# Performance work log

Measured on AMD Instinct MI355X. Metric: run time of the kernel, lower is better.

The kernel has to match this reference:

```python
import jax, jax.numpy as jnp
import numpy as np

F = 128          # num_features
NRBF = 20        # num_rbf_features
N_NODES = 25000
N_EDGES = 400000


def setup_inputs() -> dict:
    key = jax.random.key(0)
    ks = jax.random.split(key, 12)
    inp = {
        "idx_i": jax.random.randint(ks[0], (N_EDGES,), 0, N_NODES, dtype=jnp.int32),
        "idx_j": jax.random.randint(ks[1], (N_EDGES,), 0, N_NODES, dtype=jnp.int32),
        "rel_dir": jax.random.normal(ks[2], (N_EDGES, 3), dtype=jnp.float32),
        "rel_dist_cut": jax.random.uniform(ks[3], (N_EDGES,), dtype=jnp.float32),
        "rbf_features": jax.random.normal(ks[4], (N_EDGES, NRBF), dtype=jnp.float32),
        "scalar_features": jax.random.normal(ks[5], (N_NODES, F), dtype=jnp.float32),
        "vector_features": jax.random.normal(ks[6], (N_NODES, F, 3), dtype=jnp.float32),
        # scalar_network: Linear(F,F) -> SiLU -> Linear(F,3F)
        "W1": jax.random.normal(ks[7], (F, F), dtype=jnp.float32) / np.sqrt(F),
        "b1": jnp.zeros((F,), dtype=jnp.float32),
        "W2": jax.random.normal(ks[8], (3 * F, F), dtype=jnp.float32) / np.sqrt(F),
        "b2": jnp.zeros((3 * F,), dtype=jnp.float32),
        # rbf_network: Linear(NRBF, 3F)
        "Wr": jax.random.normal(ks[9], (3 * F, NRBF), dtype=jnp.float32) / np.sqrt(NRBF),
        "br": jnp.zeros((3 * F,), dtype=jnp.float32),
    }
    return inp


def reference(idx_i, idx_j, rel_dir, rel_dist_cut, rbf_features,
              scalar_features, vector_features, W1, b1, W2, b2, Wr, br):
    n_nodes = scalar_features.shape[0]
    # phi: per-node MLP -> [N, 3F]
    h = jax.nn.silu(scalar_features @ W1.T + b1)
    phi = h @ W2.T + b2
    # W: RBF-derived edge weights gated by cosine-cut distance -> [E, 3F]
    W = (rbf_features @ Wr.T + br) * rel_dist_cut[:, None]
    phi_W = phi[idx_j] * W                                  # [E, 3F]
    phi_W_vv, phi_W_ss, phi_W_vs = jnp.split(phi_W, 3, axis=-1)
    # scatter-add scalar residuals
    scalar_res = jax.ops.segment_sum(phi_W_ss, idx_i, num_segments=n_nodes)
    # per-edge vector messages [E, F, 3]
    vec_per_edge = (vector_features[idx_j] * phi_W_vv[..., None]
                    + phi_W_vs[..., None] * rel_dir[:, None, :])
    vector_res = jax.ops.segment_sum(vec_per_edge, idx_i, num_segments=n_nodes)
    return scalar_features + scalar_res, vector_features + vector_res
```

## Files before the change

kernel.cpp:

```cpp
#include <hip/hip_runtime.h>
#include <hip/hip_fp16.h>

#define F 128
#define F3 384
#define NRBF 20
#define NPB 16
#define CHUNK 64

typedef unsigned int u32;
typedef _Float16 half8 __attribute__((ext_vector_type(8)));
typedef float floatx4 __attribute__((ext_vector_type(4)));

__device__ __forceinline__ float2 uph(u32 u) {
    __half2 h = *(__half2*)&u;
    return __half22float2(h);
}
__device__ __forceinline__ u32 pkh(float a, float b) {
    __half2 h = __floats2half2_rn(a, b);
    return *(u32*)&h;
}

__device__ __forceinline__ float fdot2f(u32 a, u32 b, float c) {
#if defined(__has_builtin)
#if __has_builtin(__builtin_amdgcn_fdot2)
    typedef _Float16 h2 __attribute__((ext_vector_type(2)));
    return __builtin_amdgcn_fdot2(*(h2*)&a, *(h2*)&b, c, false);
#else
    float2 fa = uph(a), fb = uph(b);
    return fmaf(fa.x, fb.x, fmaf(fa.y, fb.y, c));
#endif
#else
    float2 fa = uph(a), fb = uph(b);
    return fmaf(fa.x, fb.x, fmaf(fa.y, fb.y, c));
#endif
}

__global__ void prep_kernel(const float* __restrict__ Wr,
                            const float* __restrict__ W1, const float* __restrict__ W2,
                            u32* __restrict__ WrTh, _Float16* __restrict__ Wh,
                            int* __restrict__ counts, int n_nodes) {
    int t = blockIdx.x * blockDim.x + threadIdx.x;
    if (t < 10 * F3) {
        int rr = t / F3, f = t % F3;
        WrTh[rr * F3 + f] = pkh(Wr[f * NRBF + 2 * rr], Wr[f * NRBF + 2 * rr + 1]);
        return;
    }
    int u = t - 10 * F3;
    if (u < (F + F3) * F) {
        int n = u >> 7, k = u & (F - 1);
        float w = (n < F) ? W1[n * F + k] : W2[(size_t)(n - F) * F + k];
        Wh[u] = (_Float16)w;
        return;
    }
    int z = u - (F + F3) * F;
    if (z < n_nodes) counts[z] = 0;
}

__launch_bounds__(256)
__global__ void fusedB2_kernel(const float* __restrict__ sf,
                               const _Float16* __restrict__ Wh,
                               const float* __restrict__ b1, const float* __restrict__ b2,
                               const float* __restrict__ vf, __half* __restrict__ gbufh,
                               const int* __restrict__ idx_i, int* __restrict__ counts,
                               int n_nodes, int n_edges, int PHB) {
    __shared__ _Float16 hl[4][16][136];
    int blk = blockIdx.x, tid = threadIdx.x;

    if (blk >= PHB) {
        int e = (blk - PHB) * 256 + tid;
        if (e < n_edges) atomicAdd(&counts[idx_i[e]], 1);
        return;
    }

    int lane = tid & 63;
    int wv = tid >> 6;
    int col = lane & 15;
    int kg = lane >> 4;
    int row0 = blk * 64 + wv * 16;

    half8 a1[4];
#pragma unroll
    for (int kb = 0; kb < 4; kb++) {
        int rr = row0 + col;
        if (rr >= n_nodes) rr = n_nodes - 1;
        const float4* xp = (const float4*)(sf + (size_t)rr * F + kb * 32 + kg * 8);
        float4 x0 = xp[0], x1 = xp[1];
        half8 a;
        a[0] = (_Float16)x0.x; a[1] = (_Float16)x0.y; a[2] = (_Float16)x0.z; a[3] = (_Float16)x0.w;
        a[4] = (_Float16)x1.x; a[5] = (_Float16)x1.y; a[6] = (_Float16)x1.z; a[7] = (_Float16)x1.w;
        a1[kb] = a;
    }

    floatx4 acc[8];
#pragma unroll
    for (int nt = 0; nt < 8; nt++) acc[nt] = (floatx4){0.f, 0.f, 0.f, 0.f};
#pragma unroll
    for (int nt = 0; nt < 8; nt++) {
#pragma unroll
        for (int kb = 0; kb < 4; kb++) {
            half8 b = *(const half8*)(Wh + (size_t)(nt * 16 + col) * F + kb * 32 + kg * 8);
            acc[nt] = __builtin_amdgcn_mfma_f32_16x16x32_f16(a1[kb], b, acc[nt], 0, 0, 0);
        }
    }
#pragma unroll
    for (int nt = 0; nt < 8; nt++) {
        int f1 = nt * 16 + col;
        float bb = b1[f1];
#pragma unroll
        for (int r = 0; r < 4; r++) {
            float v = acc[nt][r] + bb;
            float s = v / (1.f + __expf(-v));
            hl[wv][kg * 4 + r][f1] = (_Float16)s;
        }
    }

    half8 a2[4];
#pragma unroll
    for (int kb = 0; kb < 4; kb++)
        a2[kb] = *(const half8*)&hl[wv][col][kb * 32 + kg * 8];

#pragma unroll
    for (int c = 0; c < 3; c++) {
#pragma unroll
        for (int nt = 0; nt < 8; nt++) acc[nt] = (floatx4){0.f, 0.f, 0.f, 0.f};
#pragma unroll
        for (int nt = 0; nt < 8; nt++) {
#pragma unroll
            for (int kb = 0; kb < 4; kb++) {
                half8 b = *(const half8*)(Wh + (size_t)(F + c * 128 + nt * 16 + col) * F + kb * 32 + kg * 8);
                acc[nt] = __builtin_amdgcn_mfma_f32_16x16x32_f16(a2[kb], b, acc[nt], 0, 0, 0);
            }
        }
#pragma unroll
        for (int nt = 0; nt < 8; nt++) {
            int f2 = c * 128 + nt * 16 + col;
            float bb = b2[f2];
            int slot = (f2 & 63) * 12 + ((f2 >> 6) & 1) * 6 + (f2 >> 7);
#pragma unroll
            for (int r = 0; r < 4; r++) {
                int node = row0 + kg * 4 + r;
                if (node < n_nodes)
                    gbufh[(size_t)node * 768 + slot] = __float2half(acc[nt][r] + bb);
            }
        }
    }

    int base = blk * 64;
    for (int idx = tid; idx < 64 * 64; idx += 256) {
        int nl = idx >> 6, ln = idx & 63;
        int node = base + nl;
        if (node < n_nodes) {
            const float* v = vf + (size_t)node * F3;
            u32* gp = (u32*)(gbufh + (size_t)node * 768 + ln * 12);
            float a0 = v[ln * 3 + 0], a1v = v[ln * 3 + 1], a2v = v[ln * 3 + 2];
            float c0 = v[(ln + 64) * 3 + 0], c1 = v[(ln + 64) * 3 + 1], c2 = v[(ln + 64) * 3 + 2];
            ((__half*)gp)[3] = __float2half(a0);
            gp[2] = pkh(a1v, a2v);
            ((__half*)gp)[9] = __float2half(c0);
            gp[5] = pkh(c1, c2);
        }
    }
}

#define SCAN_T 1024
#define SCAN_MAXN 25600
__launch_bounds__(SCAN_T)
__global__ void scan_lds_kernel(const int* __restrict__ counts, int* __restrict__ row_start,
                                int* __restrict__ cursor, int n) {
    __shared__ int sbuf[SCAN_MAXN];
    __shared__ int partial[SCAN_T];
    int t = threadIdx.x;
    for (int i = t; i < n; i += SCAN_T) sbuf[i] = counts[i];
    __syncthreads();
    int C = (n + SCAN_T - 1) / SCAN_T;
    int beg = t * C, end = min(beg + C, n);
    int sum = 0;
    for (int i = beg; i < end; i++) sum += sbuf[i];
    partial[t] = sum;
    __syncthreads();
    for (int off = 1; off < SCAN_T; off <<= 1) {
        int v = (t >= off) ? partial[t - off] : 0;
        __syncthreads();
        partial[t] += v;
        __syncthreads();
    }
    int base = (t == 0) ? 0 : partial[t - 1];
    for (int i = beg; i < end; i++) { int c = sbuf[i]; sbuf[i] = base; base += c; }
    __syncthreads();
    for (int i = t; i < n; i += SCAN_T) { int v = sbuf[i]; row_start[i] = v; cursor[i] = v; }
    if (t == SCAN_T - 1) row_start[n] = partial[SCAN_T - 1];
}

__launch_bounds__(1024)
__global__ void scan_kernel(const int* __restrict__ counts, int* __restrict__ row_start,
                            int* __restrict__ cursor, int n) {
    __shared__ int partial[1024];
    int t = threadIdx.x;
    int C = (n + 1023) / 1024;
    int beg = t * C, end = min(beg + C, n);
    int sum = 0;
    for (int i = beg; i < end; i++) sum += counts[i];
    partial[t] = sum;
    __syncthreads();
    for (int off = 1; off < 1024; off <<= 1) {
        int v = (t >= off) ? partial[t - off] : 0;
        __syncthreads();
        partial[t] += v;
        __syncthreads();
    }
    int base = (t == 0) ? 0 : partial[t - 1];
    for (int i = beg; i < end; i++) {
        int c = counts[i];
        row_start[i] = base; cursor[i] = base; base += c;
    }
    if (t == 1023) row_start[n] = partial[1023];
}

__global__ void build_records(const int* __restrict__ idx_i, const int* __restrict__ idx_j,
                              const float* __restrict__ rel_dir, const float* __restrict__ rdc,
                              const float* __restrict__ rbf, int* __restrict__ cursor,
                              u32* __restrict__ recs, int n_edges) {
    int e = blockIdx.x * blockDim.x + threadIdx.x;
    if (e >= n_edges) return;
    int p = atomicAdd(&cursor[idx_i[e]], 1);
    u32 r[16];
    r[0] = (u32)idx_j[e];
    r[1] = __float_as_uint(rdc[e]);
    r[2] = __float_as_uint(rel_dir[e * 3 + 0]);
    r[3] = __float_as_uint(rel_dir[e * 3 + 1]);
    r[4] = __float_as_uint(rel_dir[e * 3 + 2]);
    const float* rb = rbf + (size_t)e * NRBF;
#pragma unroll
    for (int t = 0; t < 10; t++) r[5 + t] = pkh(rb[2 * t], rb[2 * t + 1]);
    r[15] = 0;
    float4* dst = (float4*)(recs + (size_t)p * 16);
    const float4* src = (const float4*)r;
    dst[0] = src[0]; dst[1] = src[1]; dst[2] = src[2]; dst[3] = src[3];
}

__global__ void scatter_kernel(const int* __restrict__ idx_i, int* __restrict__ cursor,
                               int* __restrict__ edge_order, int n_edges) {
    int e = blockIdx.x * blockDim.x + threadIdx.x;
    if (e < n_edges) {
        int p = atomicAdd(&cursor[idx_i[e]], 1);
        edge_order[p] = e;
    }
}

__launch_bounds__(256)
__global__ void gather5_kernel(const float* __restrict__ sf, const float* __restrict__ vf,
                               const u32* __restrict__ WrTh, const float* __restrict__ br,
                               const u32* __restrict__ gbuf, const u32* __restrict__ recs,
                               const int* __restrict__ row_start,
                               float* __restrict__ out_s, float* __restrict__ out_v,
                               int n_nodes) {
    __shared__ u32 lsm[4][CHUNK * 16];
    int tid = threadIdx.x;
    int lane = tid & 63;
    int wvid = tid >> 6;
    int w = wvid & 1;
    int node = blockIdx.x * 2 + (wvid >> 1);
    if (node >= n_nodes) return;
    u32* lds = lsm[wvid];

    int fb = lane + 64 * w;
    u32 wrpk[3][10];
    float brv[3];
#pragma unroll
    for (int k = 0; k < 3; k++) {
        brv[k] = br[fb + 128 * k];
#pragma unroll
        for (int rr = 0; rr < 10; rr++)
            wrpk[k][rr] = WrTh[rr * F3 + fb + 128 * k];
    }

    float acc_s = 0.f, av0 = 0.f, av1 = 0.f, av2 = 0.f;
    int beg = row_start[node];
    int end = row_start[node + 1];

    for (int cb = beg; cb < end; cb += CHUNK) {
        int cnt = min(CHUNK, end - cb);
        {
            const float4* src = (const float4*)(recs + (size_t)cb * 16);
            int nf4 = cnt * 4;
            for (int t = lane; t < nf4; t += 64)
                ((float4*)lds)[t] = src[t];
        }

        auto issueL = [&](u32& g0, u32& g1, u32& g2, int m) {
            if (m < cnt) {
                int j = (int)lds[m * 16];
                const u32* gp = gbuf + (size_t)j * 384 + lane * 6 + w * 3;
                g0 = gp[0]; g1 = gp[1]; g2 = gp[2];
            }
        };
        auto computeE = [&](u32 g0, u32 g1, u32 g2, int m) {
            const uint4* q = (const uint4*)(lds + m * 16);
            uint4 q0 = q[0], q1 = q[1], q2 = q[2], q3 = q[3];
            float rd = __uint_as_float(q0.y);
            float dx = __uint_as_float(q0.z);
            float dy = __uint_as_float(q0.w);
            float dz = __uint_as_float(q1.x);
            u32 rbu[10] = { q1.y, q1.z, q1.w, q2.x, q2.y, q2.z, q2.w, q3.x, q3.y, q3.z };
            float W0 = brv[0], W1f = brv[1], W2f = brv[2];
#pragma unroll
            for (int rr = 0; rr < 10; rr++) {
                W0  = fdot2f(rbu[rr], wrpk[0][rr], W0);
                W1f = fdot2f(rbu[rr], wrpk[1][rr], W1f);
                W2f = fdot2f(rbu[rr], wrpk[2][rr], W2f);
            }
            float2 p01  = uph(g0);
            float2 p2v0 = uph(g1);
            float2 v12  = uph(g2);
            float pw0 = W0  * rd * p01.x;
            float pw1 = W1f * rd * p01.y;
            float pw2 = W2f * rd * p2v0.x;
            acc_s += pw1;
            av0 += p2v0.y * pw0 + pw2 * dx;
            av1 += v12.x  * pw0 + pw2 * dy;
            av2 += v12.y  * pw0 + pw2 * dz;
        };

        u32 A0, A1, A2, B0, B1, B2, C0, C1, C2, D0, D1, D2;
        issueL(A0, A1, A2, 0); issueL(B0, B1, B2, 1);
        issueL(C0, C1, C2, 2); issueL(D0, D1, D2, 3);
        int m = 0;
        while (true) {
            if (m >= cnt) break; computeE(A0, A1, A2, m); m++; issueL(A0, A1, A2, m + 3);
            if (m >= cnt) break; computeE(B0, B1, B2, m); m++; issueL(B0, B1, B2, m + 3);
            if (m >= cnt) break; computeE(C0, C1, C2, m); m++; issueL(C0, C1, C2, m + 3);
            if (m >= cnt) break; computeE(D0, D1, D2, m); m++; issueL(D0, D1, D2, m + 3);
        }
    }

    out_s[(size_t)node * F + fb] = sf[(size_t)node * F + fb] + acc_s;
    const float* vfi = vf + (size_t)node * F3 + fb * 3;
    float* ovi = out_v + (size_t)node * F3 + fb * 3;
    ovi[0] = vfi[0] + av0;
    ovi[1] = vfi[1] + av1;
    ovi[2] = vfi[2] + av2;
}

__launch_bounds__(256)
__global__ void gather3_kernel(const int* __restrict__ idx_j,
                               const float* __restrict__ rel_dir, const float* __restrict__ rdc,
                               const float* __restrict__ rbf,
                               const float* __restrict__ sf, const float* __restrict__ vf,
                               const u32* __restrict__ WrTh, const float* __restrict__ br,
                               const u32* __restrict__ gbuf,
                               const int* __restrict__ row_start, const int* __restrict__ edge_order,
                               float* __restrict__ out_s, float* __restrict__ out_v,
                               int n_nodes) {
    int lane = threadIdx.x & 63;
    int w = (threadIdx.x >> 6) & 1;
    int node = blockIdx.x * 2 + (threadIdx.x >> 7);
    if (node >= n_nodes) return;

    int fb = lane + 64 * w;
    u32 wrpk[3][10];
    float brv[3];
#pragma unroll
    for (int k = 0; k < 3; k++) {
        brv[k] = br[fb + 128 * k];
#pragma unroll
        for (int rr = 0; rr < 10; rr++)
            wrpk[k][rr] = WrTh[rr * F3 + fb + 128 * k];
    }

    float acc_s = 0.f, av0 = 0.f, av1 = 0.f, av2 = 0.f;
    int beg = row_start[node];
    int end = row_start[node + 1];

    for (int cb = beg; cb < end; cb += 64) {
        int cnt = min(64, end - cb);
        int jv = 0; float rdv = 0.f, dxv = 0.f, dyv = 0.f, dzv = 0.f;
        u32 rbm[10];
#pragma unroll
        for (int rr = 0; rr < 10; rr++) rbm[rr] = 0;
        if (lane < cnt) {
            int e = edge_order[cb + lane];
            jv = idx_j[e];
            rdv = rdc[e];
            dxv = rel_dir[e * 3 + 0]; dyv = rel_dir[e * 3 + 1]; dzv = rel_dir[e * 3 + 2];
            const float4* rp = (const float4*)(rbf + (size_t)e * NRBF);
            float4 r0 = rp[0], r1 = rp[1], r2 = rp[2], r3 = rp[3], r4 = rp[4];
            rbm[0] = pkh(r0.x, r0.y); rbm[1] = pkh(r0.z, r0.w);
            rbm[2] = pkh(r1.x, r1.y); rbm[3] = pkh(r1.z, r1.w);
            rbm[4] = pkh(r2.x, r2.y); rbm[5] = pkh(r2.z, r2.w);
            rbm[6] = pkh(r3.x, r3.y); rbm[7] = pkh(r3.z, r3.w);
            rbm[8] = pkh(r4.x, r4.y); rbm[9] = pkh(r4.z, r4.w);
        }
        auto issue = [&](u32& g0, u32& g1, u32& g2, int k) {
            int j = __shfl(jv, k, 64);
            const u32* gp = gbuf + (size_t)j * 384 + lane * 6 + w * 3;
            g0 = gp[0]; g1 = gp[1]; g2 = gp[2];
        };
        auto compute = [&](u32 g0, u32 g1, u32 g2, int k) {
            float rd = __shfl(rdv, k, 64);
            float dx = __shfl(dxv, k, 64);
            float dy = __shfl(dyv, k, 64);
            float dz = __shfl(dzv, k, 64);
            float W0 = brv[0], W1f = brv[1], W2f = brv[2];
#pragma unroll
            for (int rr = 0; rr < 10; rr++) {
                u32 rbi = (u32)__shfl((int)rbm[rr], k, 64);
                W0  = fdot2f(rbi, wrpk[0][rr], W0);
                W1f = fdot2f(rbi, wrpk[1][rr], W1f);
                W2f = fdot2f(rbi, wrpk[2][rr], W2f);
            }
            float2 p01 = uph(g0);
            float2 p2v0 = uph(g1);
            float2 v12 = uph(g2);
            float pw0 = W0 * rd * p01.x;
            float pw1 = W1f * rd * p01.y;
            float pw2 = W2f * rd * p2v0.x;
            acc_s += pw1;
            av0 += p2v0.y * pw0 + pw2 * dx;
            av1 += v12.x  * pw0 + pw2 * dy;
            av2 += v12.y  * pw0 + pw2 * dz;
        };
        u32 A0, A1, A2, B0, B1, B2;
        issue(A0, A1, A2, 0);
        int k = 0;
        while (k + 2 <= cnt) {
            issue(B0, B1, B2, k + 1);
            compute(A0, A1, A2, k);
            if (k + 2 < cnt) issue(A0, A1, A2, k + 2);
            compute(B0, B1, B2, k + 1);
            k += 2;
        }
        if (k < cnt) compute(A0, A1, A2, k);
    }

    out_s[(size_t)node * F + fb] = sf[(size_t)node * F + fb] + acc_s;
    const float* vfi = vf + (size_t)node * F3 + fb * 3;
    float* ovi = out_v + (size_t)node * F3 + fb * 3;
    ovi[0] = vfi[0] + av0;
    ovi[1] = vfi[1] + av1;
    ovi[2] = vfi[2] + av2;
}

__global__ void transpose_wr(const float* __restrict__ Wr, float* __restrict__ WrT) {
    int idx = blockIdx.x * blockDim.x + threadIdx.x;
    if (idx < F3 * NRBF) {
        int f = idx / NRBF, r = idx % NRBF;
        WrT[r * F3 + f] = Wr[idx];
    }
}

__global__ void init_out(const float* __restrict__ sf, const float* __restrict__ vf,
                         float* __restrict__ out, int n_scalar, int n_total) {
    int i = blockIdx.x * blockDim.x + threadIdx.x;
    int n4 = n_total >> 2;
    if (i < n4) {
        float4 v;
        int base = i << 2;
        if (base < n_scalar) v = ((const float4*)sf)[i];
        else                 v = ((const float4*)vf)[i - (n_scalar >> 2)];
        ((float4*)out)[i] = v;
    }
}

__launch_bounds__(256)
__global__ void phi32_kernel(const float* __restrict__ sf,
                             const float* __restrict__ W1, const float* __restrict__ b1,
                             const float* __restrict__ W2, const float* __restrict__ b2,
                             float* __restrict__ phi, int n_nodes) {
    __shared__ float xs[NPB][F];
    __shared__ float hs[NPB][F];
    int tid = threadIdx.x;
    int nb = blockIdx.x * NPB;
    for (int t = tid; t < NPB * F / 4; t += 256) {
        int n  = t / (F / 4);
        int k4 = t % (F / 4);
        float4 v = make_float4(0.f, 0.f, 0.f, 0.f);
        if (nb + n < n_nodes) v = ((const float4*)(sf + (size_t)(nb + n) * F))[k4];
        ((float4*)&xs[n][0])[k4] = v;
    }
    __syncthreads();
    {
        int f = tid & (F - 1);
        int half_ = tid >> 7;
        float acc[8];
#pragma unroll
        for (int nn = 0; nn < 8; nn++) acc[nn] = 0.f;
        const float* w1row = W1 + (size_t)f * F;
        for (int k = 0; k < F; k++) {
            float w = w1row[k];
#pragma unroll
            for (int nn = 0; nn < 8; nn++)
                acc[nn] += xs[half_ * 8 + nn][k] * w;
        }
        float b = b1[f];
#pragma unroll
        for (int nn = 0; nn < 8; nn++) {
            float v = acc[nn] + b;
            hs[half_ * 8 + nn][f] = v / (1.f + __expf(-v));
        }
    }
    __syncthreads();
    for (int f = tid; f < F3; f += 256) {
        float acc[NPB];
#pragma unroll
        for (int n = 0; n < NPB; n++) acc[n] = 0.f;
        const float* w2row = W2 + (size_t)f * F;
        for (int k = 0; k < F; k++) {
            float w = w2row[k];
#pragma unroll
            for (int n = 0; n < NPB; n++)
                acc[n] += hs[n][k] * w;
        }
        float b = b2[f];
        for (int n = 0; n < NPB; n++)
            if (nb + n < n_nodes)
                phi[(size_t)(nb + n) * F3 + f] = acc[n] + b;
    }
}

__launch_bounds__(256)
__global__ void edge_kernel(const int* __restrict__ idx_i, const int* __restrict__ idx_j,
                            const float* __restrict__ rel_dir, const float* __restrict__ rdc,
                            const float* __restrict__ rbf,
                            const float* __restrict__ vf,
                            const float* __restrict__ WrT, const float* __restrict__ br,
                            const float* __restrict__ phi,
                            float* __restrict__ out_s, float* __restrict__ out_v,
                            int n_edges) {
    int lane = threadIdx.x & 63;
    int e = (int)((blockIdx.x * (unsigned)blockDim.x + threadIdx.x) >> 6);
    if (e >= n_edges) return;
    int i = idx_i[e], j = idx_j[e];
    float rd = rdc[e];
    float d0 = rel_dir[e * 3 + 0], d1 = rel_dir[e * 3 + 1], d2 = rel_dir[e * 3 + 2];
    float rb[NRBF];
#pragma unroll
    for (int r = 0; r < NRBF; r++) rb[r] = rbf[(size_t)e * NRBF + r];
    const float* pj = phi + (size_t)j * F3;
    float pw[6];
#pragma unroll
    for (int q = 0; q < 6; q++) {
        int f = lane + 64 * q;
        float acc = br[f];
#pragma unroll
        for (int r = 0; r < NRBF; r++)
            acc += rb[r] * WrT[r * F3 + f];
        pw[q] = acc * rd * pj[f];
    }
    atomicAdd(&out_s[(size_t)i * F + lane],       pw[2]);
    atomicAdd(&out_s[(size_t)i * F + lane + 64],  pw[3]);
    const float* vfj = vf + (size_t)j * F * 3;
    float* ovi = out_v + (size_t)i * F * 3;
#pragma unroll
    for (int h = 0; h < 2; h++) {
        int f = lane + 64 * h;
        float vv = pw[h];
        float vs = pw[4 + h];
        atomicAdd(&ovi[f * 3 + 0], vfj[f * 3 + 0] * vv + vs * d0);
        atomicAdd(&ovi[f * 3 + 1], vfj[f * 3 + 1] * vv + vs * d1);
        atomicAdd(&ovi[f * 3 + 2], vfj[f * 3 + 2] * vv + vs * d2);
    }
}

extern "C" void kernel_launch(void* const* d_in, const int* in_sizes, int n_in,
                              void* d_out, int out_size, void* d_ws, size_t ws_size,
                              hipStream_t stream) {
    const int*   idx_i   = (const int*)d_in[0];
    const int*   idx_j   = (const int*)d_in[1];
    const float* rel_dir = (const float*)d_in[2];
    const float* rdc     = (const float*)d_in[3];
    const float* rbf     = (const float*)d_in[4];
    const float* sf      = (const float*)d_in[5];
    const float* vf      = (const float*)d_in[6];
    const float* W1      = (const float*)d_in[7];
    const float* b1      = (const float*)d_in[8];
    const float* W2      = (const float*)d_in[9];
    const float* b2      = (const float*)d_in[10];
    const float* Wr      = (const float*)d_in[11];
    const float* br      = (const float*)d_in[12];

    int E = in_sizes[0];
    int N = in_sizes[5] / F;

    float* out_s = (float*)d_out;
    float* out_v = out_s + (size_t)N * F;

    size_t off = 0;
    auto slab = [&](size_t bytes) { size_t o = off; off = (off + bytes + 255) & ~(size_t)255; return o; };
    size_t o_wrth = slab((size_t)10 * F3 * sizeof(u32));
    size_t o_wh   = slab((size_t)(F + F3) * F * sizeof(_Float16));
    size_t o_gbuf = slab((size_t)N * 768 * sizeof(__half));
    size_t o_cnt  = slab((size_t)N * sizeof(int));
    size_t o_row  = slab((size_t)(N + 1) * sizeof(int));
    size_t o_rec  = slab((size_t)E * 64);
    size_t need_v5 = off;

    size_t off3 = 0;
    auto slab3 = [&](size_t bytes) { size_t o = off3; off3 = (off3 + bytes + 255) & ~(size_t)255; return o; };
    size_t t_wrth = slab3((size_t)10 * F3 * sizeof(u32));
    size_t t_wh   = slab3((size_t)(F + F3) * F * sizeof(_Float16));
    size_t t_gbuf = slab3((size_t)N * 768 * sizeof(__half));
    size_t t_cnt  = slab3((size_t)N * sizeof(int));
    size_t t_row  = slab3((size_t)(N + 1) * sizeof(int));
    size_t t_ord  = slab3((size_t)E * sizeof(int));
    size_t need_v3 = off3;

    int prep_threads = 10 * F3 + (F + F3) * F + N;
    int HB = (E + 255) / 256;
    int PHB = (N + 63) / 64;

    if (ws_size >= need_v5) {
        u32*      WrTh      = (u32*)((char*)d_ws + o_wrth);
        _Float16* Wh        = (_Float16*)((char*)d_ws + o_wh);
        __half*   gbufh     = (__half*)((char*)d_ws + o_gbuf);
        u32*      gbuf      = (u32*)gbufh;
        int*      counts    = (int*)((char*)d_ws + o_cnt);
        int*      cursor    = counts;
        int*      row_start = (int*)((char*)d_ws + o_row);
        u32*      recs      = (u32*)((char*)d_ws + o_rec);

        prep_kernel<<<(prep_threads + 255) / 256, 256, 0, stream>>>(Wr, W1, W2, WrTh, Wh, counts, N);
        fusedB2_kernel<<<PHB + HB, 256, 0, stream>>>(sf, Wh, b1, b2, vf, gbufh,
                                                     idx_i, counts, N, E, PHB);
        if (N <= SCAN_MAXN)
            scan_lds_kernel<<<1, SCAN_T, 0, stream>>>(counts, row_start, cursor, N);
        else
            scan_kernel<<<1, 1024, 0, stream>>>(counts, row_start, cursor, N);
        build_records<<<(E + 255) / 256, 256, 0, stream>>>(idx_i, idx_j, rel_dir, rdc, rbf,
                                                           cursor, recs, E);
        gather5_kernel<<<(N + 1) / 2, 256, 0, stream>>>(sf, vf, WrTh, br, gbuf, recs,
                                                        row_start, out_s, out_v, N);
    } else if (ws_size >= need_v3) {
        u32*      WrTh      = (u32*)((char*)d_ws + t_wrth);
        _Float16* Wh        = (_Float16*)((char*)d_ws + t_wh);
        __half*   gbufh     = (__half*)((char*)d_ws + t_gbuf);
        u32*      gbuf      = (u32*)gbufh;
        int*      counts    = (int*)((char*)d_ws + t_cnt);
        int*      cursor    = counts;
        int*      row_start = (int*)((char*)d_ws + t_row);
        int*      edge_ord  = (int*)((char*)d_ws + t_ord);

        prep_kernel<<<(prep_threads + 255) / 256, 256, 0, stream>>>(Wr, W1, W2, WrTh, Wh, counts, N);
        fusedB2_kernel<<<PHB + HB, 256, 0, stream>>>(sf, Wh, b1, b2, vf, gbufh,
                                                     idx_i, counts, N, E, PHB);
        if (N <= SCAN_MAXN)
            scan_lds_kernel<<<1, SCAN_T, 0, stream>>>(counts, row_start, cursor, N);
        else
            scan_kernel<<<1, 1024, 0, stream>>>(counts, row_start, cursor, N);
        scatter_kernel<<<(E + 255) / 256, 256, 0, stream>>>(idx_i, cursor, edge_ord, E);
        gather3_kernel<<<(N + 1) / 2, 256, 0, stream>>>(idx_j, rel_dir, rdc, rbf, sf, vf,
                                                        WrTh, br, gbuf, row_start, edge_ord,
                                                        out_s, out_v, N);
    } else {
        size_t off2 = 0;
        auto slab2 = [&](size_t bytes) { size_t o = off2; off2 = (off2 + bytes + 255) & ~(size_t)255; return o; };
        size_t f_wrt = slab2((size_t)F3 * NRBF * sizeof(float));
        size_t f_phi = slab2((size_t)N * F3 * sizeof(float));
        float* WrT = (float*)((char*)d_ws + f_wrt);
        float* phi = (float*)((char*)d_ws + f_phi);

        int n_scalar = N * F;
        int n_total  = N * F * 4;
        init_out<<<(n_total / 4 + 255) / 256, 256, 0, stream>>>(sf, vf, (float*)d_out, n_scalar, n_total);
        transpose_wr<<<(F3 * NRBF + 255) / 256, 256, 0, stream>>>(Wr, WrT);
        phi32_kernel<<<(N + NPB - 1) / NPB, 256, 0, stream>>>(sf, W1, b1, W2, b2, phi, N);
        edge_kernel<<<(E + 3) / 4, 256, 0, stream>>>(idx_i, idx_j, rel_dir, rdc, rbf,
                                                     vf, WrT, br, phi, out_s, out_v, E);
    }
}
```

Baseline: 233.6 us.

## Process each node with one wavefront covering two features per lane

The gather kernel now assigns one 64-lane wavefront per destination node instead of two. Each lane handles features lane and lane+64, so the per-edge record in LDS and the edge loop are shared across twice the work. Each lane now issues 8-byte gbuf loads instead of 4-byte ones, and the edge-record LDS copy is done once per node instead of twice. In exchange, register pressure roughly doubles (60 packed Wr weights per lane), which may reduce occupancy, and there are half as many wavefronts to hide gather latency.

Result: slower. 260.8 us (+11.6%).

```diff
diff --git a/kernel.cpp b/kernel.cpp
--- a/kernel.cpp
+++ b/kernel.cpp
@@ -247,8 +247,10 @@
     }
 }
 
+struct Gb { uint2 a, b, c; };
+
 __launch_bounds__(256)
-__global__ void gather5_kernel(const float* __restrict__ sf, const float* __restrict__ vf,
+__global__ void gather6_kernel(const float* __restrict__ sf, const float* __restrict__ vf,
                                const u32* __restrict__ WrTh, const float* __restrict__ br,
                                const u32* __restrict__ gbuf, const u32* __restrict__ recs,
                                const int* __restrict__ row_start,
@@ -258,23 +260,28 @@
     int tid = threadIdx.x;
     int lane = tid & 63;
     int wvid = tid >> 6;
-    int w = wvid & 1;
-    int node = blockIdx.x * 2 + (wvid >> 1);
+    int node = blockIdx.x * 4 + wvid;
     if (node >= n_nodes) return;
     u32* lds = lsm[wvid];
 
-    int fb = lane + 64 * w;
-    u32 wrpk[3][10];
-    float brv[3];
-#pragma unroll
-    for (int k = 0; k < 3; k++) {
-        brv[k] = br[fb + 128 * k];
-#pragma unroll
-        for (int rr = 0; rr < 10; rr++)
-            wrpk[k][rr] = WrTh[rr * F3 + fb + 128 * k];
-    }
-
-    float acc_s = 0.f, av0 = 0.f, av1 = 0.f, av2 = 0.f;
+    u32 wrpk[6][10];
+    float brv[6];
+    {
+        const int fofs[6] = { 0, 128, 256, 64, 192, 320 };
+#pragma unroll
+        for (int k = 0; k < 6; k++) {
+            int f = lane + fofs[k];
+            brv[k] = br[f];
+#pragma unroll
+            for (int rr = 0; rr < 10; rr++)
+                wrpk[k][rr] = WrTh[rr * F3 + f];
+        }
+    }
+
+    float accs0 = 0.f, accs1 = 0.f;
+    float avA0 = 0.f, avA1 = 0.f, avA2 = 0.f;
+    float avB0 = 0.f, avB1 = 0.f, avB2 = 0.f;
+
     int beg = row_start[node];
     int end = row_start[node + 1];
 
@@ -287,14 +294,16 @@
                 ((float4*)lds)[t] = src[t];
         }
 
-        auto issueL = [&](u32& g0, u32& g1, u32& g2, int m) {
+        auto issueL = [&](Gb& g, int m) {
             if (m < cnt) {
                 int j = (int)lds[m * 16];
-                const u32* gp = gbuf + (size_t)j * 384 + lane * 6 + w * 3;
-                g0 = gp[0]; g1 = gp[1]; g2 = gp[2];
+                const u32* gp = gbuf + (size_t)j * 384 + lane * 6;
+                g.a = *(const uint2*)gp;
+                g.b = *(const uint2*)(gp + 2);
+                g.c = *(const uint2*)(gp + 4);
             }
         };
-        auto computeE = [&](u32 g0, u32 g1, u32 g2, int m) {
+        auto computeE = [&](const Gb& g, int m) {
             const uint4* q = (const uint4*)(lds + m * 16);
             uint4 q0 = q[0], q1 = q[1], q2 = q[2], q3 = q[3];
             float rd = __uint_as_float(q0.y);
@@ -302,43 +311,57 @@
             float dy = __uint_as_float(q0.w);
             float dz = __uint_as_float(q1.x);
             u32 rbu[10] = { q1.y, q1.z, q1.w, q2.x, q2.y, q2.z, q2.w, q3.x, q3.y, q3.z };
-            float W0 = brv[0], W1f = brv[1], W2f = brv[2];
-#pragma unroll
-            for (int rr = 0; rr < 10; rr++) {
-                W0  = fdot2f(rbu[rr], wrpk[0][rr], W0);
-                W1f = fdot2f(rbu[rr], wrpk[1][rr], W1f);
-                W2f = fdot2f(rbu[rr], wrpk[2][rr], W2f);
+            float W[6];
+#pragma unroll
+            for (int k = 0; k < 6; k++) {
+                float acc = brv[k];
+#pragma unroll
+                for (int rr = 0; rr < 10; rr++)
+                    acc = fdot2f(rbu[rr], wrpk[k][rr], acc);
+                W[k] = acc * rd;
             }
-            float2 p01  = uph(g0);
-            float2 p2v0 = uph(g1);
-            float2 v12  = uph(g2);
-            float pw0 = W0  * rd * p01.x;
-            float pw1 = W1f * rd * p01.y;
-            float pw2 = W2f * rd * p2v0.x;
-            acc_s += pw1;
-            av0 += p2v0.y * pw0 + pw2 * dx;
-            av1 += v12.x  * pw0 + pw2 * dy;
-            av2 += v12.y  * pw0 + pw2 * dz;
+            float2 pA = uph(g.a.x);
+            float2 pB = uph(g.a.y);
+            float2 pC = uph(g.b.x);
+            float2 pD = uph(g.b.y);
+            float2 pE = uph(g.c.x);
+            float2 pF = uph(g.c.y);
+            float pwvA = W[0] * pA.x, pwsA = W[1] * pA.y, pwxA = W[2] * pB.x;
+            float pwvB = W[3] * pD.x, pwsB = W[4] * pD.y, pwxB = W[5] * pE.x;
+            accs0 += pwsA;
+            accs1 += pwsB;
+            avA0 += pB.y * pwvA + pwxA * dx;
+            avA1 += pC.x * pwvA + pwxA * dy;
+            avA2 += pC.y * pwvA + pwxA * dz;
+            avB0 += pE.y * pwvB + pwxB * dx;
+            avB1 += pF.x * pwvB + pwxB * dy;
+            avB2 += pF.y * pwvB + pwxB * dz;
         };
 
-        u32 A0, A1, A2, B0, B1, B2, C0, C1, C2, D0, D1, D2;
-        issueL(A0, A1, A2, 0); issueL(B0, B1, B2, 1);
-        issueL(C0, C1, C2, 2); issueL(D0, D1, D2, 3);
+        Gb A, B, C, D;
+        issueL(A, 0); issueL(B, 1); issueL(C, 2); issueL(D, 3);
         int m = 0;
         while (true) {
-            if (m >= cnt) break; computeE(A0, A1, A2, m); m++; issueL(A0, A1, A2, m + 3);
-            if (m >= cnt) break; computeE(B0, B1, B2, m); m++; issueL(B0, B1, B2, m + 3);
-            if (m >= cnt) break; computeE(C0, C1, C2, m); m++; issueL(C0, C1, C2, m + 3);
-            if (m >= cnt) break; computeE(D0, D1, D2, m); m++; issueL(D0, D1, D2, m + 3);
-        }
-    }
-
-    out_s[(size_t)node * F + fb] = sf[(size_t)node * F + fb] + acc_s;
-    const float* vfi = vf + (size_t)node * F3 + fb * 3;
-    float* ovi = out_v + (size_t)node * F3 + fb * 3;
-    ovi[0] = vfi[0] + av0;
-    ovi[1] = vfi[1] + av1;
-    ovi[2] = vfi[2] + av2;
+            if (m >= cnt) break; computeE(A, m); m++; issueL(A, m + 3);
+            if (m >= cnt) break; computeE(B, m); m++; issueL(B, m + 3);
+            if (m >= cnt) break; computeE(C, m); m++; issueL(C, m + 3);
+            if (m >= cnt) break; computeE(D, m); m++; issueL(D, m + 3);
+        }
+    }
+
+    const float* sfi = sf + (size_t)node * F;
+    float* osi = out_s + (size_t)node * F;
+    osi[lane]      = sfi[lane]      + accs0;
+    osi[lane + 64] = sfi[lane + 64] + accs1;
+
+    const float* vfi = vf + (size_t)node * F3;
+    float* ovi = out_v + (size_t)node * F3;
+    ovi[lane * 3 + 0] = vfi[lane * 3 + 0] + avA0;
+    ovi[lane * 3 + 1] = vfi[lane * 3 + 1] + avA1;
+    ovi[lane * 3 + 2] = vfi[lane * 3 + 2] + avA2;
+    ovi[(lane + 64) * 3 + 0] = vfi[(lane + 64) * 3 + 0] + avB0;
+    ovi[(lane + 64) * 3 + 1] = vfi[(lane + 64) * 3 + 1] + avB1;
+    ovi[(lane + 64) * 3 + 2] = vfi[(lane + 64) * 3 + 2] + avB2;
 }
 
 __launch_bounds__(256)
@@ -627,7 +650,7 @@
             scan_kernel<<<1, 1024, 0, stream>>>(counts, row_start, cursor, N);
         build_records<<<(E + 255) / 256, 256, 0, stream>>>(idx_i, idx_j, rel_dir, rdc, rbf,
                                                            cursor, recs, E);
-        gather5_kernel<<<(N + 1) / 2, 256, 0, stream>>>(sf, vf, WrTh, br, gbuf, recs,
+        gather6_kernel<<<(N + 3) / 4, 256, 0, stream>>>(sf, vf, WrTh, br, gbuf, recs,
                                                         row_start, out_s, out_v, N);
     } else if (ws_size >= need_v3) {
         u32*      WrTh      = (u32*)((char*)d_ws + t_wrth);
```
